# Kernel tuning notes

Measured on AMD Instinct MI355X. Metric: run time of the kernel, lower is better.

The kernel has to match this reference:

```python
import jax, jax.numpy as jnp
import numpy as np


def setup_inputs() -> dict:
    key = jax.random.key(0)
    k1, k2, k3, k4 = jax.random.split(key, 4)
    B, S, IN, H = 4, 2048, 512, 1024
    x = jax.random.normal(k1, (B, S, IN), dtype=jnp.float32)
    W1 = jax.random.normal(k2, (IN, H), dtype=jnp.float32) * (1.0 / np.sqrt(IN))
    b1 = jax.random.normal(k3, (H,), dtype=jnp.float32) * 0.02
    Wq = jax.random.normal(k4, (H, H), dtype=jnp.float32) * (1.0 / np.sqrt(H))
    return {"x": x, "W1": W1, "b1": b1, "Wq": Wq, "atten_size": 16}


def reference(x, W1, b1, Wq, atten_size):
    A = atten_size
    B, S, _ = x.shape
    H = W1.shape[1]
    h = jax.nn.relu(jnp.einsum('bsi,ih->bsh', x, W1) + b1)  # [B,S,H]
    # zero-pad sequence dim by A on each side
    padded = jnp.pad(h, ((0, 0), (A, A), (0, 0)))  # [B,S+2A,H]
    # torch: stack(roll(padded, k, 1) for k in -A..A, dim=2) then slice [A:-A]
    # => x_nei[b, i, j] = padded[b, 2A + i - j]
    idx = 2 * A + jnp.arange(S)[:, None] - jnp.arange(2 * A + 1)[None, :]  # [S,W]
    x_nei = padded[:, idx, :]  # [B,S,W,H]
    q = jnp.einsum('bsh,hk->bsk', h, Wq)  # [B,S,H]
    scores = jnp.einsum('bsh,bswh->bsw', q, x_nei) / jnp.sqrt(jnp.asarray(H, x.dtype))
    w = jax.nn.softmax(scores, axis=2)  # softmax over window axis
    out = jnp.einsum('bsw,bswh->bsh', w, x_nei)
    return out
```

## Files before the change

### kernel.cpp

```cpp
#include <hip/hip_runtime.h>
#include <stdint.h>

constexpr int BATCH = 4;
constexpr int SEQ   = 2048;
constexpr int DIN   = 512;
constexpr int DH    = 1024;
constexpr int BS    = BATCH * SEQ;
constexpr int AP    = 32;
constexpr int AW    = 64;

typedef float  floatx4 __attribute__((ext_vector_type(4)));
typedef short  bf16x8  __attribute__((ext_vector_type(8)));

static __device__ __forceinline__ unsigned short f2bf(float f) {
  union { float f; unsigned u; } v; v.f = f;
  unsigned r = (v.u + 0x7fffu + ((v.u >> 16) & 1u)) >> 16;
  return (unsigned short)r;
}

static __device__ __forceinline__ void gld_lds16(const unsigned short* g, const short* l) {
  typedef const __attribute__((address_space(1))) void* gvp;
  typedef __attribute__((address_space(3))) void* lvp;
  __builtin_amdgcn_global_load_lds((gvp)(uintptr_t)g, (lvp)(unsigned)(uintptr_t)l, 16, 0, 0);
}

__global__ __launch_bounds__(256) void prep_k(const float* __restrict__ X,
                                              const float* __restrict__ W1,
                                              const float* __restrict__ Wq,
                                              unsigned short* __restrict__ Xb,
                                              unsigned short* __restrict__ w1t,
                                              unsigned short* __restrict__ wqt) {
  __shared__ float t[32][33];
  if (blockIdx.y >= 48) {
    const int t0 = ((blockIdx.y - 48) * 32 + blockIdx.x) * 256 + threadIdx.x;
    const float4 a = ((const float4*)X)[(size_t)t0 * 2];
    const float4 b = ((const float4*)X)[(size_t)t0 * 2 + 1];
    __align__(16) unsigned short o[8];
    o[0] = f2bf(a.x); o[1] = f2bf(a.y); o[2] = f2bf(a.z); o[3] = f2bf(a.w);
    o[4] = f2bf(b.x); o[5] = f2bf(b.y); o[6] = f2bf(b.z); o[7] = f2bf(b.w);
    *(uint4*)(Xb + (size_t)t0 * 8) = *(const uint4*)o;
    return;
  }
  const bool isW1 = blockIdx.y < 16;
  const float* in = isW1 ? W1 : Wq;
  unsigned short* out = isW1 ? w1t : wqt;
  const int R = isW1 ? DIN : DH;
  const int C = DH;
  const int r0 = (isW1 ? blockIdx.y : (blockIdx.y - 16)) * 32;
  const int c0 = blockIdx.x * 32;
  const int tx = threadIdx.x & 31, ty = threadIdx.x >> 5;
  for (int i = ty; i < 32; i += 8) t[i][tx] = in[(size_t)(r0 + i) * C + c0 + tx];
  __syncthreads();
  for (int i = ty; i < 32; i += 8) out[(size_t)(c0 + i) * R + r0 + tx] = f2bf(t[tx][i]);
}

__global__ __launch_bounds__(256) void gemm_k(const unsigned short* __restrict__ Ab,
                                              const unsigned short* __restrict__ Bt,
                                              const float* __restrict__ bias,
                                              unsigned short* __restrict__ outB,
                                              unsigned short* __restrict__ outBT,
                                              const int K) {
  const int M = BS, N = DH;
  __shared__ __align__(16) short As[2][2][128 * 32];
  const int tid = threadIdx.x;
  const int f   = blockIdx.x;
  const int t   = (f & 7) * 64 + (f >> 3);
  const int m0  = (t & 63) * 128, n0 = (t >> 6) * 128;
  const int wv  = tid >> 6, lane = tid & 63;
  const int wm  = (wv >> 1) * 64, wn = (wv & 1) * 64;
  const int l16 = lane & 15, quad = lane >> 4;
  const int ra  = lane >> 2, ca = (lane & 3) * 8;

  const unsigned short* gA  = Ab + (size_t)(m0 + wv * 32 + ra) * K + ca;
  const unsigned short* gB0 = Bt + (size_t)(n0 + wn + l16) * K + quad * 8;

  floatx4 acc[4][4];
  for (int i = 0; i < 4; i++)
    for (int j = 0; j < 4; j++) acc[i][j] = {0.f, 0.f, 0.f, 0.f};

  bf16x8 b0[2][4], b1[2][4];

  auto stageA = [&](int tb, int ks) {
    const unsigned short* a = gA + ks * 64;
    short* la = &As[tb][0][wv * 1024];
    gld_lds16(a, la);
    gld_lds16(a + 16 * K, la + 512);
    short* lb = &As[tb][1][wv * 1024];
    gld_lds16(a + 32, lb);
    gld_lds16(a + 16 * K + 32, lb + 512);
  };

#define LOADB(dst, ks)                                                          \
  _Pragma("unroll") for (int h = 0; h < 2; h++)                                 \
  _Pragma("unroll") for (int j = 0; j < 4; j++)                                 \
      dst[h][j] = *(const bf16x8*)(gB0 + (size_t)(j * 16) * K + (ks) * 64 + h * 32);

#define COMPUTE(tb, bb)                                                         \
  {                                                                             \
    bf16x8 af[4];                                                               \
    _Pragma("unroll") for (int h = 0; h < 2; h++) {                             \
      _Pragma("unroll") for (int i = 0; i < 4; i++)                             \
          af[i] = *(const bf16x8*)&As[tb][h][(wm + i * 16 + l16) * 32 + quad * 8]; \
      __builtin_amdgcn_s_setprio(1);                                            \
      _Pragma("unroll") for (int i = 0; i < 4; i++)                             \
      _Pragma("unroll") for (int j = 0; j < 4; j++)                             \
          acc[i][j] = __builtin_amdgcn_mfma_f32_16x16x32_bf16(af[i], bb[h][j],  \
                                                              acc[i][j], 0, 0, 0); \
      __builtin_amdgcn_s_setprio(0);                                            \
    }                                                                           \
  }

  const int NK = K / 64;
  LOADB(b0, 0);
  stageA(0, 0);
  __syncthreads();
  for (int ks = 0; ks < NK; ks += 2) {
    LOADB(b1, ks + 1);
    stageA(1, ks + 1);
    COMPUTE(0, b0);
    __syncthreads();
    if (ks + 2 < NK) {
      LOADB(b0, ks + 2);
      stageA(0, ks + 2);
    }
    COMPUTE(1, b1);
    __syncthreads();
  }
#undef LOADB
#undef COMPUTE

  for (int j = 0; j < 4; j++) {
    const int col = n0 + wn + j * 16 + l16;
    const float bv = bias ? bias[col] : 0.f;
    for (int i = 0; i < 4; i++) {
      const int rowb = m0 + wm + i * 16 + quad * 4;
      float v[4];
      for (int r = 0; r < 4; r++) {
        float x = acc[i][j][r] + bv;
        v[r] = bias ? fmaxf(x, 0.f) : x;
      }
      for (int r = 0; r < 4; r++) outB[(size_t)(rowb + r) * N + col] = f2bf(v[r]);
      if (outBT) {
        ushort4 o4; o4.x = f2bf(v[0]); o4.y = f2bf(v[1]); o4.z = f2bf(v[2]); o4.w = f2bf(v[3]);
        *(ushort4*)(outBT + (size_t)col * M + rowb) = o4;
      }
    }
  }
}

__global__ __launch_bounds__(1024) void attn_mfma_k(const unsigned short* __restrict__ hb,
                                                    const unsigned short* __restrict__ hbT,
                                                    const unsigned short* __restrict__ qb,
                                                    float* __restrict__ out) {
  __shared__ float Sf[2][32 * 64];
  __shared__ __align__(16) short Ps[32 * 72];

  const int tid  = threadIdx.x;
  const int wave = tid >> 6, lane = tid & 63;
  const int l16  = lane & 15, quad = lane >> 4;
  const int p0   = blockIdx.x * AP;
  const int s0   = p0 & (SEQ - 1);

  for (int i = tid; i < 32 * 72 / 2; i += 1024) ((unsigned*)Ps)[i] = 0;

  {
    const int kh = wave & 1;
    const int nt = (wave >> 1) & 3;
    const int mt = wave >> 3;
    const unsigned short* qp = qb + (size_t)(p0 + mt * 16 + l16) * DH + kh * 512 + quad * 8;
    const int hrow = s0 - 16 + nt * 16 + l16;
    const bool hv = (hrow >= 0) && (hrow < SEQ);
    const unsigned short* hp = hb + (long long)(p0 - 16 + nt * 16 + l16) * DH + kh * 512 + quad * 8;

    floatx4 ac[4] = {{0,0,0,0},{0,0,0,0},{0,0,0,0},{0,0,0,0}};
    const bf16x8 hz = {0,0,0,0,0,0,0,0};
    __builtin_amdgcn_s_setprio(1);
    #pragma unroll
    for (int it = 0; it < 16; ++it) {
      bf16x8 qa = *(const bf16x8*)(qp + it * 32);
      bf16x8 ha = hz;
      if (hv) ha = *(const bf16x8*)(hp + it * 32);
      ac[it & 3] = __builtin_amdgcn_mfma_f32_16x16x32_bf16(qa, ha, ac[it & 3], 0, 0, 0);
    }
    __builtin_amdgcn_s_setprio(0);
    floatx4 s4;
    for (int r = 0; r < 4; r++)
      s4[r] = (ac[0][r] + ac[1][r]) + (ac[2][r] + ac[3][r]);
    for (int r = 0; r < 4; r++)
      Sf[kh][(mt * 16 + quad * 4 + r) * 64 + nt * 16 + l16] = s4[r] * (1.f / 32.f);
  }
  __syncthreads();

  if (tid < 512) {
    const int row = tid >> 4, k = tid & 15;
    const float v0 = Sf[0][row * 64 + row + k] + Sf[1][row * 64 + row + k];
    const float v1 = Sf[0][row * 64 + row + k + 16] + Sf[1][row * 64 + row + k + 16];
    const float v2 = (k == 0) ? (Sf[0][row * 64 + row + 32] + Sf[1][row * 64 + row + 32]) : -1e30f;
    float mx = fmaxf(v0, fmaxf(v1, v2));
    for (int off = 1; off < 16; off <<= 1) mx = fmaxf(mx, __shfl_xor(mx, off, 64));
    const float e0 = __expf(v0 - mx), e1 = __expf(v1 - mx);
    const float e2 = (k == 0) ? __expf(v2 - mx) : 0.f;
    float sum = e0 + e1 + e2;
    for (int off = 1; off < 16; off <<= 1) sum += __shfl_xor(sum, off, 64);
    const float inv = 1.f / sum;
    Ps[row * 72 + row + k] = f2bf(e0 * inv);
    Ps[row * 72 + row + k + 16] = f2bf(e1 * inv);
    if (k == 0) Ps[row * 72 + row + 32] = f2bf(e2 * inv);
  }
  __syncthreads();

  {
    const bf16x8 pb00 = *(const bf16x8*)&Ps[(l16) * 72 + quad * 8];
    const bf16x8 pb01 = *(const bf16x8*)&Ps[(l16) * 72 + 32 + quad * 8];
    const bf16x8 pb10 = *(const bf16x8*)&Ps[(16 + l16) * 72 + quad * 8];
    const bf16x8 pb11 = *(const bf16x8*)&Ps[(16 + l16) * 72 + 32 + quad * 8];

    int lo = 16 - s0; if (lo < 0) lo = 0;
    int hi = SEQ + 16 - s0; if (hi > AW) hi = AW;
    const bool interior = (lo == 0) && (hi == AW);

    #pragma unroll
    for (int i = 0; i < 4; ++i) {
      const int mt2 = wave * 4 + i;
      const unsigned short* ap = hbT + (size_t)(mt2 * 16 + l16) * BS + (p0 - 16) + quad * 8;
      bf16x8 aa0 = *(const bf16x8*)(ap);
      bf16x8 aa1 = *(const bf16x8*)(ap + 32);
      if (!interior) {
        #pragma unroll
        for (int j = 0; j < 8; j++) {
          const int k = quad * 8 + j;
          if (k < lo || k >= hi) aa0[j] = 0;
          if (k + 32 < lo || k + 32 >= hi) aa1[j] = 0;
        }
      }
      floatx4 o0 = {0.f, 0.f, 0.f, 0.f}, o1 = {0.f, 0.f, 0.f, 0.f};
      __builtin_amdgcn_s_setprio(1);
      o0 = __builtin_amdgcn_mfma_f32_16x16x32_bf16(aa0, pb00, o0, 0, 0, 0);
      o0 = __builtin_amdgcn_mfma_f32_16x16x32_bf16(aa1, pb01, o0, 0, 0, 0);
      o1 = __builtin_amdgcn_mfma_f32_16x16x32_bf16(aa0, pb10, o1, 0, 0, 0);
      o1 = __builtin_amdgcn_mfma_f32_16x16x32_bf16(aa1, pb11, o1, 0, 0, 0);
      __builtin_amdgcn_s_setprio(0);
      float4 s0v; s0v.x = o0[0]; s0v.y = o0[1]; s0v.z = o0[2]; s0v.w = o0[3];
      float4 s1v; s1v.x = o1[0]; s1v.y = o1[1]; s1v.z = o1[2]; s1v.w = o1[3];
      *(float4*)(out + (size_t)(p0 + l16) * DH + mt2 * 16 + quad * 4) = s0v;
      *(float4*)(out + (size_t)(p0 + 16 + l16) * DH + mt2 * 16 + quad * 4) = s1v;
    }
  }
}

extern "C" void kernel_launch(void* const* d_in, const int* in_sizes, int n_in,
                              void* d_out, int out_size, void* d_ws, size_t ws_size,
                              hipStream_t stream) {
  const float* x  = (const float*)d_in[0];
  const float* W1 = (const float*)d_in[1];
  const float* b1 = (const float*)d_in[2];
  const float* Wq = (const float*)d_in[3];

  char* w = (char*)d_ws;
  unsigned short* w1t = (unsigned short*)(w);
  unsigned short* wqt = (unsigned short*)(w + (1ull  << 20));
  unsigned short* hb  = (unsigned short*)(w + (3ull  << 20));
  unsigned short* hbT = (unsigned short*)(w + (19ull << 20));
  unsigned short* qb  = (unsigned short*)(w + (35ull << 20));
  unsigned short* xb  = qb;

  prep_k<<<dim3(32, 112), 256, 0, stream>>>(x, W1, Wq, xb, w1t, wqt);

  gemm_k<<<512, 256, 0, stream>>>(xb, w1t, b1, hb, hbT, DIN);
  gemm_k<<<512, 256, 0, stream>>>(hb, wqt, nullptr, qb, nullptr, DH);

  attn_mfma_k<<<BS / AP, 1024, 0, stream>>>(hb, hbT, qb, (float*)d_out);
}
```

Baseline: 187.3 us.

## Stage B tiles through LDS and template GEMM on K and epilogue flags

The GEMM now loads the B operand into shared memory with async global-to-LDS copies, matching how A is handled, instead of each wave reading B fragments straight from global into registers. The pipeline becomes a single double-buffered loop with explicit vmcnt waits and raw barriers. K, ReLU and the transposed-output store become template parameters, so loop trip counts and epilogue branches are known at compile time. The grid changes from a swizzled 1D launch to a plain 2D grid, which drops the L2-friendly block ordering and doubles LDS use per block.

```diff
diff --git a/kernel.cpp b/kernel.cpp
--- a/kernel.cpp
+++ b/kernel.cpp
@@ -54,93 +54,82 @@
   for (int i = ty; i < 32; i += 8) out[(size_t)(c0 + i) * R + r0 + tx] = f2bf(t[tx][i]);
 }
 
+template <int K, bool RELU, bool WT>
 __global__ __launch_bounds__(256) void gemm_k(const unsigned short* __restrict__ Ab,
                                               const unsigned short* __restrict__ Bt,
                                               const float* __restrict__ bias,
                                               unsigned short* __restrict__ outB,
-                                              unsigned short* __restrict__ outBT,
-                                              const int K) {
+                                              unsigned short* __restrict__ outBT) {
   const int M = BS, N = DH;
   __shared__ __align__(16) short As[2][2][128 * 32];
-  const int tid = threadIdx.x;
-  const int f   = blockIdx.x;
-  const int t   = (f & 7) * 64 + (f >> 3);
-  const int m0  = (t & 63) * 128, n0 = (t >> 6) * 128;
-  const int wv  = tid >> 6, lane = tid & 63;
-  const int wm  = (wv >> 1) * 64, wn = (wv & 1) * 64;
-  const int l16 = lane & 15, quad = lane >> 4;
-  const int ra  = lane >> 2, ca = (lane & 3) * 8;
-
-  const unsigned short* gA  = Ab + (size_t)(m0 + wv * 32 + ra) * K + ca;
-  const unsigned short* gB0 = Bt + (size_t)(n0 + wn + l16) * K + quad * 8;
+  __shared__ __align__(16) short Bs[2][2][128 * 32];
+  const int tid  = threadIdx.x;
+  const int m0   = blockIdx.x * 128, n0 = blockIdx.y * 128;
+  const int wv   = tid >> 6, lane = tid & 63;
+  const int wm   = (wv >> 1) * 64, wn = (wv & 1) * 64;
+  const int l16  = lane & 15, quad = lane >> 4;
+  const int ra   = lane >> 2, ca = (lane & 3) * 8;
+
+  const unsigned short* gA = Ab + (size_t)(m0 + wv * 32 + ra) * K + ca;
+  const unsigned short* gB = Bt + (size_t)(n0 + wv * 32 + ra) * K + ca;
 
   floatx4 acc[4][4];
   for (int i = 0; i < 4; i++)
     for (int j = 0; j < 4; j++) acc[i][j] = {0.f, 0.f, 0.f, 0.f};
 
-  bf16x8 b0[2][4], b1[2][4];
-
-  auto stageA = [&](int tb, int ks) {
+  auto stage = [&](int buf, int ks) {
     const unsigned short* a = gA + ks * 64;
-    short* la = &As[tb][0][wv * 1024];
-    gld_lds16(a, la);
-    gld_lds16(a + 16 * K, la + 512);
-    short* lb = &As[tb][1][wv * 1024];
-    gld_lds16(a + 32, lb);
-    gld_lds16(a + 16 * K + 32, lb + 512);
+    const unsigned short* b = gB + ks * 64;
+    gld_lds16(a,               &As[buf][0][wv * 1024]);
+    gld_lds16(a + 16 * K,      &As[buf][0][wv * 1024 + 512]);
+    gld_lds16(a + 32,          &As[buf][1][wv * 1024]);
+    gld_lds16(a + 16 * K + 32, &As[buf][1][wv * 1024 + 512]);
+    gld_lds16(b,               &Bs[buf][0][wv * 1024]);
+    gld_lds16(b + 16 * K,      &Bs[buf][0][wv * 1024 + 512]);
+    gld_lds16(b + 32,          &Bs[buf][1][wv * 1024]);
+    gld_lds16(b + 16 * K + 32, &Bs[buf][1][wv * 1024 + 512]);
   };
 
-#define LOADB(dst, ks)                                                          \
-  _Pragma("unroll") for (int h = 0; h < 2; h++)                                 \
-  _Pragma("unroll") for (int j = 0; j < 4; j++)                                 \
-      dst[h][j] = *(const bf16x8*)(gB0 + (size_t)(j * 16) * K + (ks) * 64 + h * 32);
-
-#define COMPUTE(tb, bb)                                                         \
-  {                                                                             \
-    bf16x8 af[4];                                                               \
-    _Pragma("unroll") for (int h = 0; h < 2; h++) {                             \
-      _Pragma("unroll") for (int i = 0; i < 4; i++)                             \
-          af[i] = *(const bf16x8*)&As[tb][h][(wm + i * 16 + l16) * 32 + quad * 8]; \
-      __builtin_amdgcn_s_setprio(1);                                            \
-      _Pragma("unroll") for (int i = 0; i < 4; i++)                             \
-      _Pragma("unroll") for (int j = 0; j < 4; j++)                             \
-          acc[i][j] = __builtin_amdgcn_mfma_f32_16x16x32_bf16(af[i], bb[h][j],  \
-                                                              acc[i][j], 0, 0, 0); \
-      __builtin_amdgcn_s_setprio(0);                                            \
-    }                                                                           \
-  }
-
-  const int NK = K / 64;
-  LOADB(b0, 0);
-  stageA(0, 0);
-  __syncthreads();
-  for (int ks = 0; ks < NK; ks += 2) {
-    LOADB(b1, ks + 1);
-    stageA(1, ks + 1);
-    COMPUTE(0, b0);
-    __syncthreads();
-    if (ks + 2 < NK) {
-      LOADB(b0, ks + 2);
-      stageA(0, ks + 2);
-    }
-    COMPUTE(1, b1);
-    __syncthreads();
-  }
-#undef LOADB
-#undef COMPUTE
+  constexpr int NK = K / 64;
+  stage(0, 0);
+  for (int ks = 0; ks < NK; ++ks) {
+    const int cur = ks & 1;
+    __builtin_amdgcn_s_barrier();
+    if (ks + 1 < NK) {
+      stage(cur ^ 1, ks + 1);
+      asm volatile("s_waitcnt vmcnt(8)" ::: "memory");
+    } else {
+      asm volatile("s_waitcnt vmcnt(0)" ::: "memory");
+    }
+    __builtin_amdgcn_s_barrier();
+    __builtin_amdgcn_sched_barrier(0);
+    bf16x8 af[4], bfr[4];
+    #pragma unroll
+    for (int h = 0; h < 2; h++) {
+      for (int i = 0; i < 4; i++)
+        af[i] = *(const bf16x8*)&As[cur][h][(wm + i * 16 + l16) * 32 + quad * 8];
+      for (int j = 0; j < 4; j++)
+        bfr[j] = *(const bf16x8*)&Bs[cur][h][(wn + j * 16 + l16) * 32 + quad * 8];
+      __builtin_amdgcn_s_setprio(1);
+      for (int i = 0; i < 4; i++)
+        for (int j = 0; j < 4; j++)
+          acc[i][j] = __builtin_amdgcn_mfma_f32_16x16x32_bf16(af[i], bfr[j], acc[i][j], 0, 0, 0);
+      __builtin_amdgcn_s_setprio(0);
+    }
+  }
 
   for (int j = 0; j < 4; j++) {
     const int col = n0 + wn + j * 16 + l16;
-    const float bv = bias ? bias[col] : 0.f;
+    const float bv = RELU ? bias[col] : 0.f;
     for (int i = 0; i < 4; i++) {
       const int rowb = m0 + wm + i * 16 + quad * 4;
       float v[4];
       for (int r = 0; r < 4; r++) {
         float x = acc[i][j][r] + bv;
-        v[r] = bias ? fmaxf(x, 0.f) : x;
+        v[r] = RELU ? fmaxf(x, 0.f) : x;
       }
       for (int r = 0; r < 4; r++) outB[(size_t)(rowb + r) * N + col] = f2bf(v[r]);
-      if (outBT) {
+      if (WT) {
         ushort4 o4; o4.x = f2bf(v[0]); o4.y = f2bf(v[1]); o4.z = f2bf(v[2]); o4.w = f2bf(v[3]);
         *(ushort4*)(outBT + (size_t)col * M + rowb) = o4;
       }
@@ -266,8 +255,8 @@
 
   prep_k<<<dim3(32, 112), 256, 0, stream>>>(x, W1, Wq, xb, w1t, wqt);
 
-  gemm_k<<<512, 256, 0, stream>>>(xb, w1t, b1, hb, hbT, DIN);
-  gemm_k<<<512, 256, 0, stream>>>(hb, wqt, nullptr, qb, nullptr, DH);
+  gemm_k<DIN, true, true><<<dim3(BS / 128, DH / 128), 256, 0, stream>>>(xb, w1t, b1, hb, hbT);
+  gemm_k<DH, false, false><<<dim3(BS / 128, DH / 128), 256, 0, stream>>>(hb, wqt, nullptr, qb, nullptr);
 
   attn_mfma_k<<<BS / AP, 1024, 0, stream>>>(hb, hbT, qb, (float*)d_out);
 }
```

After: 156.6 us. 16.4% less time.
